# Kernel optimization log

Measured on AMD Instinct MI355X. Metric: run time of the kernel, lower is better.

The kernel has to match this reference:

```python
import jax, jax.numpy as jnp
import numpy as np

T, B, VOCAB, HID = 256, 32, 8192, 1024


def setup_inputs() -> dict:
    key = jax.random.key(0)
    ks = jax.random.split(key, 11)
    s = 1.0 / np.sqrt(HID)  # PyTorch LSTM init: U(-1/sqrt(H), 1/sqrt(H))
    u = lambda k, shape: jax.random.uniform(k, shape, jnp.float32, -s, s)
    return {
        "x": jax.random.randint(ks[0], (T, B), 0, VOCAB),
        "H": jax.random.normal(ks[1], (2, B, HID), jnp.float32),
        "C": jax.random.normal(ks[2], (2, B, HID), jnp.float32),
        "W_ih0": u(ks[3], (4 * HID, VOCAB)),
        "W_hh0": u(ks[4], (4 * HID, HID)),
        "b_ih0": u(ks[5], (4 * HID,)),
        "b_hh0": u(ks[6], (4 * HID,)),
        "W_ih1": u(ks[7], (4 * HID, HID)),
        "W_hh1": u(ks[8], (4 * HID, HID)),
        "b_ih1": u(ks[9], (4 * HID,)),
        "b_hh1": u(ks[10], (4 * HID,)),
    }


def _lstm_layer(gx, h0, c0, W_hh):
    """gx: (T, B, 4H) precomputed input-side gates incl. both biases."""
    def step(carry, g):
        h, c = carry
        gates = g + h @ W_hh.T  # (B, 4H)
        i, f, gg, o = jnp.split(gates, 4, axis=-1)  # PyTorch gate order i,f,g,o
        c = jax.nn.sigmoid(f) * c + jax.nn.sigmoid(i) * jnp.tanh(gg)
        h = jax.nn.sigmoid(o) * jnp.tanh(c)
        return (h, c), h
    (h, c), ys = jax.lax.scan(step, (h0, c0), gx)
    return ys, h, c


def reference(x, H, C, W_ih0, W_hh0, b_ih0, b_hh0, W_ih1, W_hh1, b_ih1, b_hh1):
    # one_hot(x).float() @ W_ih0.T == row gather of W_ih0.T (identical math)
    gx0 = jnp.take(W_ih0.T, x, axis=0) + (b_ih0 + b_hh0)  # (T, B, 4H)
    y0, h0, c0 = _lstm_layer(gx0, H[0], C[0], W_hh0)
    gx1 = jnp.einsum("tbh,gh->tbg", y0, W_ih1) + (b_ih1 + b_hh1)
    y1, h1, c1 = _lstm_layer(gx1, H[1], C[1], W_hh1)
    return y1, jnp.stack([h0, h1]), jnp.stack([c0, c1])
```

## Files before the change

kernel.cpp:

```cpp
#include <hip/hip_runtime.h>

#define DI __device__ __forceinline__

using half8 = __attribute__((ext_vector_type(8))) _Float16;
using f32x4 = __attribute__((ext_vector_type(4))) float;
using ull = unsigned long long;

static constexpr int T_ = 256;
static constexpr int B_ = 32;
static constexpr int H_ = 1024;
static constexpr int V_ = 8192;
static constexpr int TPB = 256;
static constexpr int BH = B_ * H_;
static constexpr int GX = 4 * H_;
static constexpr int TC = 8;
static constexpr int NCH = T_ / TC;
static constexpr int GUARD = 60000;

__device__ _Float16 g_y0loc[(T_ + 1) * BH];
__device__ _Float16 g_y1loc[(T_ + 1) * BH];
__device__ ull g_y0pub[(size_t)(T_ + 1) * BH / 4];
__device__ _Float16 g_ggx[(size_t)T_ * B_ * GX];
__device__ _Float16 g_Wt[(size_t)V_ * GX];
__device__ unsigned g_xcdcnt[8 * 32];
__device__ unsigned g_heltick[32];
__device__ unsigned g_arr0[4 * 32], g_arr1[4 * 32];
__device__ unsigned g_ep0[32], g_ep1[32];
__device__ unsigned g_l0prog[32];
__device__ unsigned g_chunk[NCH * 32];

__global__ void init_bar_k() {
  const int i = threadIdx.x;
  if (i < 256) g_xcdcnt[i] = 0u;
  if (i < 128) { g_arr0[i] = 0u; g_arr1[i] = 0u; }
  if (i < 32)  { g_ep0[i] = 0u; g_ep1[i] = 0u; g_l0prog[i] = 0u; g_heltick[i] = 0u; }
  g_chunk[i] = 0u;
}

__global__ __launch_bounds__(256) void transpose_wih0(const float* __restrict__ in) {
  __shared__ _Float16 t[64][72];
  const int bc = blockIdx.x & 127;
  const int br = blockIdx.x >> 7;
  const int r0 = br * 64, v0 = bc * 64;
  const int tx = threadIdx.x & 15, ty = threadIdx.x >> 4;
#pragma unroll
  for (int it = 0; it < 4; ++it) {
    const int row = ty + it * 16;
    const float4 f = *(const float4*)&in[(size_t)(r0 + row) * V_ + v0 + tx * 4];
    t[tx * 4 + 0][row] = (_Float16)f.x;
    t[tx * 4 + 1][row] = (_Float16)f.y;
    t[tx * 4 + 2][row] = (_Float16)f.z;
    t[tx * 4 + 3][row] = (_Float16)f.w;
  }
  __syncthreads();
#pragma unroll
  for (int it = 0; it < 4; ++it) {
    const int vrow = ty + it * 16;
    union { _Float16 h[4]; ull u; } o;
    o.h[0] = t[vrow][tx * 4 + 0]; o.h[1] = t[vrow][tx * 4 + 1];
    o.h[2] = t[vrow][tx * 4 + 2]; o.h[3] = t[vrow][tx * 4 + 3];
    *(ull*)&g_Wt[(size_t)(v0 + vrow) * GX + r0 + tx * 4] = o.u;
  }
}

DI unsigned ld_ag(const unsigned* p) { return __hip_atomic_load(p, __ATOMIC_RELAXED, __HIP_MEMORY_SCOPE_AGENT); }
DI void st_ag(unsigned* p, unsigned v) { __hip_atomic_store(p, v, __ATOMIC_RELAXED, __HIP_MEMORY_SCOPE_AGENT); }
DI unsigned add_ag(unsigned* p) { return __hip_atomic_fetch_add(p, 1u, __ATOMIC_RELAXED, __HIP_MEMORY_SCOPE_AGENT); }
DI void st_ag64(ull* p, ull v) { __hip_atomic_store(p, v, __ATOMIC_RELAXED, __HIP_MEMORY_SCOPE_AGENT); }

DI float sigmf(float v) { return 1.0f / (1.0f + __expf(-v)); }
DI float tanhf_(float v) { return 1.0f - 2.0f / (__expf(2.0f * v) + 1.0f); }

DI half8 load8_cvt(const float* __restrict__ p) {
  const float4* q = (const float4*)p;
  float4 a = q[0], b = q[1];
  half8 r;
  r[0] = (_Float16)a.x; r[1] = (_Float16)a.y; r[2] = (_Float16)a.z; r[3] = (_Float16)a.w;
  r[4] = (_Float16)b.x; r[5] = (_Float16)b.y; r[6] = (_Float16)b.z; r[7] = (_Float16)b.w;
  return r;
}

DI void stage_h(_Float16* ldsbase, const _Float16* src, int w) {
  const int lane = (int)(threadIdx.x & 63);
#pragma unroll
  for (int i = 0; i < 16; ++i) {
    const int d = (w * 16 + i) * 64 + lane;
    const int row = d >> 7;
    const int cir = d & 127;
    const int sc = row * 128 + (cir ^ (row & 7));
    __builtin_amdgcn_global_load_lds(
        (const __attribute__((address_space(1))) void*)((const char*)src + (size_t)sc * 16),
        (__attribute__((address_space(3))) void*)((char*)ldsbase + (size_t)(w * 16 + i) * 1024),
        16, 0, 0);
  }
}

DI half8 lds_a(const _Float16* stg, int arow, int kk, int kgb) {
  unsigned off = (unsigned)(arow * 2048 + kk * 64 + kgb);
  off ^= (unsigned)((arow & 7) << 4);
  return *(const half8*)((const char*)stg + off);
}

__global__ __launch_bounds__(TPB, 1) void lstm_fused(
    const float* __restrict__ Whh0,
    const float* __restrict__ bih0, const float* __restrict__ bhh0,
    const float* __restrict__ Wih1,
    const float* __restrict__ Whh1,
    const float* __restrict__ bih1, const float* __restrict__ bhh1,
    const int* __restrict__ x,
    const float* __restrict__ Hst,
    const float* __restrict__ Cst,
    float* __restrict__ y1out,
    float* __restrict__ outh,
    float* __restrict__ outc)
{
  const int tid = threadIdx.x;
  const int lane = tid & 63;
  const int w = tid >> 6;

  __shared__ _Float16 stage_s[BH];
  __shared__ float gates_s[32 * 132];
  __shared__ unsigned sh_xcc, sh_rank;

  if (tid == 0) {
    unsigned xc;
    asm volatile("s_getreg_b32 %0, hwreg(HW_REG_XCC_ID)" : "=s"(xc));
    xc &= 7u;
    sh_xcc = xc;
    sh_rank = __hip_atomic_fetch_add(&g_xcdcnt[xc * 32], 1u,
                                     __ATOMIC_RELAXED, __HIP_MEMORY_SCOPE_AGENT);
  }
  __syncthreads();
  const unsigned xcc = sh_xcc;
  const unsigned rank = sh_rank;

  const int kgrp = (lane >> 4) * 8;
  const int kgb = (lane >> 4) * 16;

  if (xcc <= 1u && rank < 32u) {
    const bool isL1 = (xcc == 1u);
    const int jbase = (int)rank * 32;
    const float* Whh = isL1 ? Whh1 : Whh0;
    const float* bih = isL1 ? bih1 : bih0;
    const float* bhh = isL1 ? bhh1 : bhh0;
    _Float16* yloc = isL1 ? g_y1loc : g_y0loc;
    unsigned* arr = isL1 ? g_arr1 : g_arr0;
    unsigned* ep = isL1 ? g_ep1 : g_ep0;
    const int arrline = (int)(rank & 3);

    half8 wf0[32], wf1[32];
    {
      const int rw0 = w * H_ + jbase + (lane & 15);
      const int rw1 = rw0 + 16;
#pragma unroll
      for (int kk = 0; kk < 32; ++kk) {
        wf0[kk] = load8_cvt(Whh + (size_t)rw0 * H_ + kk * 32 + kgrp);
        wf1[kk] = load8_cvt(Whh + (size_t)rw1 * H_ + kk * 32 + kgrp);
      }
    }

    const int b = tid >> 3;
    const int d0 = (tid & 7) * 4;
    const int j0 = jbase + d0;

    float bs[4][4];
#pragma unroll
    for (int g = 0; g < 4; ++g)
#pragma unroll
      for (int dd = 0; dd < 4; ++dd)
        bs[g][dd] = bih[g * H_ + j0 + dd] + bhh[g * H_ + j0 + dd];

    float cc[4], hf[4];
    {
      const float4 hi = *(const float4*)&Hst[(isL1 ? BH : 0) + b * H_ + j0];
      const float4 ci = *(const float4*)&Cst[(isL1 ? BH : 0) + b * H_ + j0];
      cc[0] = ci.x; cc[1] = ci.y; cc[2] = ci.z; cc[3] = ci.w;
      hf[0] = hi.x; hf[1] = hi.y; hf[2] = hi.z; hf[3] = hi.w;
    }
    union { _Float16 h[4]; ull u; } pk;
#pragma unroll
    for (int dd = 0; dd < 4; ++dd) pk.h[dd] = (_Float16)hf[dd];
    ull hv_keep = pk.u;
    *(ull*)&yloc[(size_t)b * H_ + j0] = hv_keep;

    __syncthreads();
    if (tid == 0) add_ag(&arr[arrline * 32]);

    float h_last = hf[0];
    (void)h_last;

    for (int t = 0; t < T_; ++t) {
      ull gxu[4];
      if (!isL1) {
        const int xv = x[t * B_ + b];
        const _Float16* gp = g_Wt + (size_t)xv * GX + j0;
#pragma unroll
        for (int g = 0; g < 4; ++g) gxu[g] = *(const ull*)(gp + g * H_);
      }

      if (tid == 0) {
        const unsigned r = (unsigned)(t + 1);
        int guard = 0;
        if (rank == 0u) {
          const unsigned tgt = 8u * r;
          for (;;) {
            bool ok = true;
#pragma unroll
            for (int i = 0; i < 4; ++i) ok &= (ld_ag(&arr[i * 32]) >= tgt);
            if (isL1 && ok && (t & (TC - 1)) == 0)
              ok &= (ld_ag(&g_chunk[(t / TC) * 32]) >= 128u);
            if (ok) break;
            __builtin_amdgcn_s_sleep(1);
            if (++guard > GUARD) break;
          }
          st_ag(ep, r);
          if (!isL1 && t >= 1) st_ag(g_l0prog, (unsigned)(t - 1));
        } else {
          while (ld_ag(ep) < r) {
            __builtin_amdgcn_s_sleep(1);
            if (++guard > GUARD) break;
          }
        }
      }
      __syncthreads();

      if (isL1) {
        const _Float16* gp = g_ggx + ((size_t)t * B_ + b) * GX + j0;
#pragma unroll
        for (int g = 0; g < 4; ++g) gxu[g] = *(const ull*)(gp + g * H_);
      }

      if (!isL1)
        st_ag64(&g_y0pub[((size_t)t * BH + b * H_ + j0) >> 2], hv_keep);

      stage_h(stage_s, yloc + (size_t)t * BH, w);
      __syncthreads();

      f32x4 a00 = {0.f,0.f,0.f,0.f}, a01 = {0.f,0.f,0.f,0.f};
      f32x4 a10 = {0.f,0.f,0.f,0.f}, a11 = {0.f,0.f,0.f,0.f};
#pragma unroll
      for (int kk = 0; kk < 32; ++kk) {
        const half8 A0 = lds_a(stage_s, (lane & 15), kk, kgb);
        const half8 A1 = lds_a(stage_s, 16 + (lane & 15), kk, kgb);
        a00 = __builtin_amdgcn_mfma_f32_16x16x32_f16(A0, wf0[kk], a00, 0, 0, 0);
        a01 = __builtin_amdgcn_mfma_f32_16x16x32_f16(A0, wf1[kk], a01, 0, 0, 0);
        a10 = __builtin_amdgcn_mfma_f32_16x16x32_f16(A1, wf0[kk], a10, 0, 0, 0);
        a11 = __builtin_amdgcn_mfma_f32_16x16x32_f16(A1, wf1[kk], a11, 0, 0, 0);
      }

      {
        const int colb = w * 32 + (lane & 15);
        const int rowb = (lane >> 4) * 4;
#pragma unroll
        for (int r = 0; r < 4; ++r) {
          gates_s[(rowb + r) * 132 + colb]           = a00[r];
          gates_s[(rowb + r) * 132 + colb + 16]      = a01[r];
          gates_s[(16 + rowb + r) * 132 + colb]      = a10[r];
          gates_s[(16 + rowb + r) * 132 + colb + 16] = a11[r];
        }
      }
      __syncthreads();

      float gate[4][4];
#pragma unroll
      for (int g = 0; g < 4; ++g) {
        const _Float16* gh = (const _Float16*)&gxu[g];
#pragma unroll
        for (int dd = 0; dd < 4; ++dd)
          gate[g][dd] = gates_s[b * 132 + g * 32 + d0 + dd] + (float)gh[dd] + bs[g][dd];
      }
#pragma unroll
      for (int dd = 0; dd < 4; ++dd) {
        const float iv = sigmf(gate[0][dd]), fv = sigmf(gate[1][dd]);
        const float gv = tanhf_(gate[2][dd]), ov = sigmf(gate[3][dd]);
        cc[dd] = fv * cc[dd] + iv * gv;
        hf[dd] = ov * tanhf_(cc[dd]);
        pk.h[dd] = (_Float16)hf[dd];
      }
      hv_keep = pk.u;
      *(ull*)&yloc[(size_t)(t + 1) * BH + b * H_ + j0] = hv_keep;
      if (isL1)
        *(float4*)&y1out[(size_t)t * BH + b * H_ + j0] =
            make_float4(hf[0], hf[1], hf[2], hf[3]);

      __syncthreads();
      if (tid == 0) add_ag(&arr[arrline * 32]);
    }

    if (!isL1) {
      st_ag64(&g_y0pub[((size_t)T_ * BH + b * H_ + j0) >> 2], hv_keep);
      __syncthreads();
      if (tid == 0) add_ag(&g_arr0[arrline * 32]);
      if (rank == 0u && tid == 0) {
        const unsigned tgt = 8u * (unsigned)(T_ + 2);
        int guard = 0;
        for (;;) {
          bool ok = true;
#pragma unroll
          for (int i = 0; i < 4; ++i) ok &= (ld_ag(&g_arr0[i * 32]) >= tgt);
          if (ok) break;
          __builtin_amdgcn_s_sleep(1);
          if (++guard > GUARD) break;
        }
        st_ag(g_l0prog, (unsigned)T_);
      }
    }

    *(float4*)&outh[(isL1 ? BH : 0) + b * H_ + j0] = make_float4(hf[0], hf[1], hf[2], hf[3]);
    *(float4*)&outc[(isL1 ? BH : 0) + b * H_ + j0] = make_float4(cc[0], cc[1], cc[2], cc[3]);
    return;
  }

  __shared__ unsigned sh_hid;
  if (tid == 0) sh_hid = add_ag(g_heltick);
  __syncthreads();
  const unsigned hid = sh_hid;
  if (hid >= 128u) return;

  half8 wih0[32], wih1[32];
  {
    const int rw0 = (int)hid * 32 + (lane & 15);
    const int rw1 = rw0 + 16;
#pragma unroll
    for (int kk = 0; kk < 32; ++kk) {
      wih0[kk] = load8_cvt(Wih1 + (size_t)rw0 * H_ + kk * 32 + kgrp);
      wih1[kk] = load8_cvt(Wih1 + (size_t)rw1 * H_ + kk * 32 + kgrp);
    }
  }
  const int cg0 = (int)hid * 32 + (lane & 15);
  const int cg1 = cg0 + 16;
  const _Float16* y0pub = (const _Float16*)g_y0pub;

  for (int c = 0; c < NCH; ++c) {
    if (tid == 0) {
      int guard = 0;
      while (ld_ag(g_l0prog) < (unsigned)(c * TC + TC)) {
        __builtin_amdgcn_s_sleep(4);
        if (++guard > GUARD) break;
      }
    }
    __syncthreads();
    const int t0 = c * TC;

#pragma unroll 1
    for (int mt = 0; mt < 4; ++mt) {
      const int arow = w * 64 + mt * 16 + (lane & 15);
      const _Float16* asrc = y0pub + (size_t)(t0 + (arow >> 5) + 1) * BH +
                             (size_t)(arow & 31) * H_ + kgrp;
      f32x4 e0 = {0.f,0.f,0.f,0.f}, e1 = {0.f,0.f,0.f,0.f};
#pragma unroll
      for (int kk = 0; kk < 32; ++kk) {
        const half8 a = *(const half8*)(asrc + kk * 32);
        e0 = __builtin_amdgcn_mfma_f32_16x16x32_f16(a, wih0[kk], e0, 0, 0, 0);
        e1 = __builtin_amdgcn_mfma_f32_16x16x32_f16(a, wih1[kk], e1, 0, 0, 0);
      }
      const int mrow = w * 64 + mt * 16 + (lane >> 4) * 4;
#pragma unroll
      for (int r = 0; r < 4; ++r) {
        const int m = mrow + r;
        const int tt = t0 + (m >> 5);
        const int bb = m & 31;
        const _Float16 v0 = (_Float16)e0[r];
        const _Float16 v1 = (_Float16)e1[r];
        __hip_atomic_store((short*)&g_ggx[((size_t)tt * B_ + bb) * GX + cg0],
                           __builtin_bit_cast(short, v0),
                           __ATOMIC_RELAXED, __HIP_MEMORY_SCOPE_AGENT);
        __hip_atomic_store((short*)&g_ggx[((size_t)tt * B_ + bb) * GX + cg1],
                           __builtin_bit_cast(short, v1),
                           __ATOMIC_RELAXED, __HIP_MEMORY_SCOPE_AGENT);
      }
    }
    __syncthreads();
    if (tid == 0) add_ag(&g_chunk[c * 32]);
  }
}

extern "C" void kernel_launch(void* const* d_in, const int* in_sizes, int n_in,
                              void* d_out, int out_size, void* d_ws, size_t ws_size,
                              hipStream_t stream) {
  (void)in_sizes; (void)n_in; (void)d_ws; (void)ws_size; (void)out_size;

  const int*   x    = (const int*)  d_in[0];
  const float* Hst  = (const float*)d_in[1];
  const float* Cst  = (const float*)d_in[2];
  const float* Wih0 = (const float*)d_in[3];
  const float* Whh0 = (const float*)d_in[4];
  const float* bih0 = (const float*)d_in[5];
  const float* bhh0 = (const float*)d_in[6];
  const float* Wih1 = (const float*)d_in[7];
  const float* Whh1 = (const float*)d_in[8];
  const float* bih1 = (const float*)d_in[9];
  const float* bhh1 = (const float*)d_in[10];

  float* out   = (float*)d_out;
  float* y1out = out;
  float* outh  = out + (size_t)T_ * BH;
  float* outc  = outh + (size_t)2 * BH;

  hipLaunchKernelGGL(init_bar_k, dim3(1), dim3(1024), 0, stream);
  hipLaunchKernelGGL(transpose_wih0, dim3(8192), dim3(256), 0, stream, Wih0);
  hipLaunchKernelGGL(lstm_fused, dim3(256), dim3(TPB), 0, stream,
                     Whh0, bih0, bhh0, Wih1, Whh1, bih1, bhh1,
                     x, Hst, Cst, y1out, outh, outc);
}
```

Before: 1.471 ms.

## Replace counter+epoch barrier with per-block progress slots polled in parallel

```diff
diff --git a/kernel.cpp b/kernel.cpp
--- a/kernel.cpp
+++ b/kernel.cpp
@@ -20,20 +20,19 @@
 __device__ _Float16 g_y0loc[(T_ + 1) * BH];
 __device__ _Float16 g_y1loc[(T_ + 1) * BH];
 __device__ ull g_y0pub[(size_t)(T_ + 1) * BH / 4];
-__device__ _Float16 g_ggx[(size_t)T_ * B_ * GX];
+__device__ ull g_ggx[(size_t)T_ * B_ * GX / 4];
 __device__ _Float16 g_Wt[(size_t)V_ * GX];
 __device__ unsigned g_xcdcnt[8 * 32];
 __device__ unsigned g_heltick[32];
-__device__ unsigned g_arr0[4 * 32], g_arr1[4 * 32];
-__device__ unsigned g_ep0[32], g_ep1[32];
+__device__ unsigned g_slot0[32 * 8];
+__device__ unsigned g_slot1[32 * 8];
 __device__ unsigned g_l0prog[32];
 __device__ unsigned g_chunk[NCH * 32];
 
 __global__ void init_bar_k() {
   const int i = threadIdx.x;
-  if (i < 256) g_xcdcnt[i] = 0u;
-  if (i < 128) { g_arr0[i] = 0u; g_arr1[i] = 0u; }
-  if (i < 32)  { g_ep0[i] = 0u; g_ep1[i] = 0u; g_l0prog[i] = 0u; g_heltick[i] = 0u; }
+  if (i < 256) { g_xcdcnt[i] = 0u; g_slot0[i] = 0u; g_slot1[i] = 0u; }
+  if (i < 32)  { g_l0prog[i] = 0u; g_heltick[i] = 0u; }
   g_chunk[i] = 0u;
 }
 
@@ -67,6 +66,7 @@
 DI void st_ag(unsigned* p, unsigned v) { __hip_atomic_store(p, v, __ATOMIC_RELAXED, __HIP_MEMORY_SCOPE_AGENT); }
 DI unsigned add_ag(unsigned* p) { return __hip_atomic_fetch_add(p, 1u, __ATOMIC_RELAXED, __HIP_MEMORY_SCOPE_AGENT); }
 DI void st_ag64(ull* p, ull v) { __hip_atomic_store(p, v, __ATOMIC_RELAXED, __HIP_MEMORY_SCOPE_AGENT); }
+DI ull ld_ag64(const ull* p) { return __hip_atomic_load(p, __ATOMIC_RELAXED, __HIP_MEMORY_SCOPE_AGENT); }
 
 DI float sigmf(float v) { return 1.0f / (1.0f + __expf(-v)); }
 DI float tanhf_(float v) { return 1.0f - 2.0f / (__expf(2.0f * v) + 1.0f); }
@@ -78,6 +78,27 @@
   r[0] = (_Float16)a.x; r[1] = (_Float16)a.y; r[2] = (_Float16)a.z; r[3] = (_Float16)a.w;
   r[4] = (_Float16)b.x; r[5] = (_Float16)b.y; r[6] = (_Float16)b.z; r[7] = (_Float16)b.w;
   return r;
+}
+
+DI void slot_wait(unsigned* slots, unsigned r, const unsigned* extra,
+                  unsigned extraTgt) {
+  const int tid = threadIdx.x;
+  if (tid < 64) {
+    if (tid < 32) {
+      int guard = 0;
+      while (ld_ag(&slots[tid * 8]) < r) {
+        __builtin_amdgcn_s_sleep(1);
+        if (++guard > GUARD) break;
+      }
+    } else if (tid == 32 && extra) {
+      int guard = 0;
+      while (ld_ag(extra) < extraTgt) {
+        __builtin_amdgcn_s_sleep(1);
+        if (++guard > GUARD) break;
+      }
+    }
+  }
+  __syncthreads();
 }
 
 DI void stage_h(_Float16* ldsbase, const _Float16* src, int w) {
@@ -144,9 +165,7 @@
     const float* bih = isL1 ? bih1 : bih0;
     const float* bhh = isL1 ? bhh1 : bhh0;
     _Float16* yloc = isL1 ? g_y1loc : g_y0loc;
-    unsigned* arr = isL1 ? g_arr1 : g_arr0;
-    unsigned* ep = isL1 ? g_ep1 : g_ep0;
-    const int arrline = (int)(rank & 3);
+    unsigned* slots = isL1 ? g_slot1 : g_slot0;
 
     half8 wf0[32], wf1[32];
     {
@@ -184,10 +203,7 @@
     *(ull*)&yloc[(size_t)b * H_ + j0] = hv_keep;
 
     __syncthreads();
-    if (tid == 0) add_ag(&arr[arrline * 32]);
-
-    float h_last = hf[0];
-    (void)h_last;
+    if (tid == 0) st_ag(&slots[rank * 8], 1u);
 
     for (int t = 0; t < T_; ++t) {
       ull gxu[4];
@@ -196,42 +212,26 @@
         const _Float16* gp = g_Wt + (size_t)xv * GX + j0;
 #pragma unroll
         for (int g = 0; g < 4; ++g) gxu[g] = *(const ull*)(gp + g * H_);
-      }
-
-      if (tid == 0) {
-        const unsigned r = (unsigned)(t + 1);
-        int guard = 0;
-        if (rank == 0u) {
-          const unsigned tgt = 8u * r;
-          for (;;) {
-            bool ok = true;
-#pragma unroll
-            for (int i = 0; i < 4; ++i) ok &= (ld_ag(&arr[i * 32]) >= tgt);
-            if (isL1 && ok && (t & (TC - 1)) == 0)
-              ok &= (ld_ag(&g_chunk[(t / TC) * 32]) >= 128u);
-            if (ok) break;
-            __builtin_amdgcn_s_sleep(1);
-            if (++guard > GUARD) break;
-          }
-          st_ag(ep, r);
-          if (!isL1 && t >= 1) st_ag(g_l0prog, (unsigned)(t - 1));
-        } else {
-          while (ld_ag(ep) < r) {
-            __builtin_amdgcn_s_sleep(1);
-            if (++guard > GUARD) break;
-          }
-        }
-      }
-      __syncthreads();
-
-      if (isL1) {
-        const _Float16* gp = g_ggx + ((size_t)t * B_ + b) * GX + j0;
-#pragma unroll
-        for (int g = 0; g < 4; ++g) gxu[g] = *(const ull*)(gp + g * H_);
-      }
-
-      if (!isL1)
+      } else if (t & (TC - 1)) {
+        const size_t gbase = (((size_t)t * B_ + b) * GX + j0) >> 2;
+#pragma unroll
+        for (int g = 0; g < 4; ++g) gxu[g] = ld_ag64(&g_ggx[gbase + (size_t)(g * H_ >> 2)]);
+      }
+
+      const unsigned r = (unsigned)(t + 1);
+      if (isL1 && (t & (TC - 1)) == 0)
+        slot_wait(slots, r, &g_chunk[(t / TC) * 32], 128u);
+      else
+        slot_wait(slots, r, nullptr, 0u);
+
+      if (!isL1) {
+        if (rank == 0u && tid == 0 && t >= 1) st_ag(g_l0prog, (unsigned)(t - 1));
         st_ag64(&g_y0pub[((size_t)t * BH + b * H_ + j0) >> 2], hv_keep);
+      } else if ((t & (TC - 1)) == 0) {
+        const size_t gbase = (((size_t)t * B_ + b) * GX + j0) >> 2;
+#pragma unroll
+        for (int g = 0; g < 4; ++g) gxu[g] = ld_ag64(&g_ggx[gbase + (size_t)(g * H_ >> 2)]);
+      }
 
       stage_h(stage_s, yloc + (size_t)t * BH, w);
       __syncthreads();
@@ -252,27 +252,27 @@
         const int colb = w * 32 + (lane & 15);
         const int rowb = (lane >> 4) * 4;
 #pragma unroll
-        for (int r = 0; r < 4; ++r) {
-          gates_s[(rowb + r) * 132 + colb]           = a00[r];
-          gates_s[(rowb + r) * 132 + colb + 16]      = a01[r];
-          gates_s[(16 + rowb + r) * 132 + colb]      = a10[r];
-          gates_s[(16 + rowb + r) * 132 + colb + 16] = a11[r];
+        for (int r2 = 0; r2 < 4; ++r2) {
+          gates_s[(rowb + r2) * 132 + colb]           = a00[r2];
+          gates_s[(rowb + r2) * 132 + colb + 16]      = a01[r2];
+          gates_s[(16 + rowb + r2) * 132 + colb]      = a10[r2];
+          gates_s[(16 + rowb + r2) * 132 + colb + 16] = a11[r2];
         }
       }
       __syncthreads();
 
-      float gate[4][4];
-#pragma unroll
-      for (int g = 0; g < 4; ++g) {
-        const _Float16* gh = (const _Float16*)&gxu[g];
-#pragma unroll
-        for (int dd = 0; dd < 4; ++dd)
-          gate[g][dd] = gates_s[b * 132 + g * 32 + d0 + dd] + (float)gh[dd] + bs[g][dd];
-      }
+      float4 G[4];
+#pragma unroll
+      for (int g = 0; g < 4; ++g)
+        G[g] = *(const float4*)&gates_s[b * 132 + g * 32 + d0];
 #pragma unroll
       for (int dd = 0; dd < 4; ++dd) {
-        const float iv = sigmf(gate[0][dd]), fv = sigmf(gate[1][dd]);
-        const float gv = tanhf_(gate[2][dd]), ov = sigmf(gate[3][dd]);
+        const float gi = ((const float*)&G[0])[dd] + (float)((const _Float16*)&gxu[0])[dd] + bs[0][dd];
+        const float gf = ((const float*)&G[1])[dd] + (float)((const _Float16*)&gxu[1])[dd] + bs[1][dd];
+        const float gg = ((const float*)&G[2])[dd] + (float)((const _Float16*)&gxu[2])[dd] + bs[2][dd];
+        const float go = ((const float*)&G[3])[dd] + (float)((const _Float16*)&gxu[3])[dd] + bs[3][dd];
+        const float iv = sigmf(gi), fv = sigmf(gf);
+        const float gv = tanhf_(gg), ov = sigmf(go);
         cc[dd] = fv * cc[dd] + iv * gv;
         hf[dd] = ov * tanhf_(cc[dd]);
         pk.h[dd] = (_Float16)hf[dd];
@@ -284,25 +284,16 @@
             make_float4(hf[0], hf[1], hf[2], hf[3]);
 
       __syncthreads();
-      if (tid == 0) add_ag(&arr[arrline * 32]);
+      if (tid == 0) st_ag(&slots[rank * 8], (unsigned)(t + 2));
     }
 
     if (!isL1) {
       st_ag64(&g_y0pub[((size_t)T_ * BH + b * H_ + j0) >> 2], hv_keep);
       __syncthreads();
-      if (tid == 0) add_ag(&g_arr0[arrline * 32]);
-      if (rank == 0u && tid == 0) {
-        const unsigned tgt = 8u * (unsigned)(T_ + 2);
-        int guard = 0;
-        for (;;) {
-          bool ok = true;
-#pragma unroll
-          for (int i = 0; i < 4; ++i) ok &= (ld_ag(&g_arr0[i * 32]) >= tgt);
-          if (ok) break;
-          __builtin_amdgcn_s_sleep(1);
-          if (++guard > GUARD) break;
-        }
-        st_ag(g_l0prog, (unsigned)T_);
+      if (tid == 0) st_ag(&g_slot0[rank * 8], (unsigned)(T_ + 2));
+      if (rank == 0u) {
+        slot_wait(g_slot0, (unsigned)(T_ + 2), nullptr, 0u);
+        if (tid == 0) st_ag(g_l0prog, (unsigned)T_);
       }
     }
 
@@ -329,7 +320,7 @@
   }
   const int cg0 = (int)hid * 32 + (lane & 15);
   const int cg1 = cg0 + 16;
-  const _Float16* y0pub = (const _Float16*)g_y0pub;
+  short* ggx_s = (short*)g_ggx;
 
   for (int c = 0; c < NCH; ++c) {
     if (tid == 0) {
@@ -345,14 +336,16 @@
 #pragma unroll 1
     for (int mt = 0; mt < 4; ++mt) {
       const int arow = w * 64 + mt * 16 + (lane & 15);
-      const _Float16* asrc = y0pub + (size_t)(t0 + (arow >> 5) + 1) * BH +
-                             (size_t)(arow & 31) * H_ + kgrp;
+      const size_t abase = (((size_t)(t0 + (arow >> 5) + 1) * BH) +
+                            (size_t)(arow & 31) * H_ + kgrp) >> 2;
       f32x4 e0 = {0.f,0.f,0.f,0.f}, e1 = {0.f,0.f,0.f,0.f};
 #pragma unroll
       for (int kk = 0; kk < 32; ++kk) {
-        const half8 a = *(const half8*)(asrc + kk * 32);
-        e0 = __builtin_amdgcn_mfma_f32_16x16x32_f16(a, wih0[kk], e0, 0, 0, 0);
-        e1 = __builtin_amdgcn_mfma_f32_16x16x32_f16(a, wih1[kk], e1, 0, 0, 0);
+        union { ull u[2]; half8 v; } a;
+        a.u[0] = ld_ag64(&g_y0pub[abase + kk * 8]);
+        a.u[1] = ld_ag64(&g_y0pub[abase + kk * 8 + 1]);
+        e0 = __builtin_amdgcn_mfma_f32_16x16x32_f16(a.v, wih0[kk], e0, 0, 0, 0);
+        e1 = __builtin_amdgcn_mfma_f32_16x16x32_f16(a.v, wih1[kk], e1, 0, 0, 0);
       }
       const int mrow = w * 64 + mt * 16 + (lane >> 4) * 4;
 #pragma unroll
@@ -362,10 +355,10 @@
         const int bb = m & 31;
         const _Float16 v0 = (_Float16)e0[r];
         const _Float16 v1 = (_Float16)e1[r];
-        __hip_atomic_store((short*)&g_ggx[((size_t)tt * B_ + bb) * GX + cg0],
+        __hip_atomic_store(&ggx_s[((size_t)tt * B_ + bb) * GX + cg0],
                            __builtin_bit_cast(short, v0),
                            __ATOMIC_RELAXED, __HIP_MEMORY_SCOPE_AGENT);
-        __hip_atomic_store((short*)&g_ggx[((size_t)tt * B_ + bb) * GX + cg1],
+        __hip_atomic_store(&ggx_s[((size_t)tt * B_ + bb) * GX + cg1],
                            __builtin_bit_cast(short, v1),
                            __ATOMIC_RELAXED, __HIP_MEMORY_SCOPE_AGENT);
       }
```

New measurement: 1.417 ms, median of 3. 3.7% less time.
